# Kernel optimization log

Hardware: AMD Instinct MI355X
Metric: run time of the kernel (lower is better)

## Reference

```python
import jax, jax.numpy as jnp
import numpy as np

N = 50000
E = 800000
D = 128
L = 3


def gru_cell(m, h, w_ih, w_hh, b_ih, b_hh):
    # m, h: [N, D]; w_ih, w_hh: [3D, D]; b_ih, b_hh: [3D]
    gi = m @ w_ih.T + b_ih  # [N, 3D]
    gh = h @ w_hh.T + b_hh  # [N, 3D]
    i_r, i_z, i_n = jnp.split(gi, 3, axis=-1)
    h_r, h_z, h_n = jnp.split(gh, 3, axis=-1)
    r = jax.nn.sigmoid(i_r + h_r)
    z = jax.nn.sigmoid(i_z + h_z)
    n = jnp.tanh(i_n + r * h_n)
    return (1.0 - z) * n + z * h


def setup_inputs() -> dict:
    key = jax.random.key(0)
    ks = jax.random.split(key, 8)
    s = 1.0 / np.sqrt(D)
    z = jax.random.normal(ks[0], (N, D), dtype=jnp.float32)
    edge_index = jax.random.randint(ks[1], (2, E), 0, N, dtype=jnp.int64)
    weight = jax.random.uniform(ks[2], (L, D, D), dtype=jnp.float32, minval=-s, maxval=s)
    w_ih = jax.random.uniform(ks[3], (3 * D, D), dtype=jnp.float32, minval=-s, maxval=s)
    w_hh = jax.random.uniform(ks[4], (3 * D, D), dtype=jnp.float32, minval=-s, maxval=s)
    b_ih = jax.random.uniform(ks[5], (3 * D,), dtype=jnp.float32, minval=-s, maxval=s)
    b_hh = jax.random.uniform(ks[6], (3 * D,), dtype=jnp.float32, minval=-s, maxval=s)
    return {"z": z, "edge_index": edge_index, "weight": weight,
            "w_ih": w_ih, "w_hh": w_hh, "b_ih": b_ih, "b_hh": b_hh}


def reference(z, edge_index, weight, w_ih, w_hh, b_ih, b_hh):
    # GatedGraphConv: per layer, m = h @ W_l; aggregate m[src] into dst (sum); GRU update.
    src, dst = edge_index[0], edge_index[1]
    h = z  # in_channels == out_channels, no padding
    for l in range(L):
        m = h @ weight[l]                              # [N, D]
        agg = jax.ops.segment_sum(m[src], dst, num_segments=N)  # scatter-add over edges
        h = gru_cell(agg, h, w_ih, w_hh, b_ih, b_hh)
    return h
```

## Files before the change

kernel.cpp:

```cpp
#include <hip/hip_runtime.h>
#include <hip/hip_bf16.h>

#define NN 50000
#define NE 800000
#define D 128
#define NL 3
#define G3 384

typedef __attribute__((ext_vector_type(4))) float f32x4;
typedef __attribute__((ext_vector_type(2))) float f32x2;
typedef _Float16 f16;
typedef __attribute__((ext_vector_type(8))) _Float16 f16x8;
typedef __attribute__((ext_vector_type(2))) _Float16 f16x2;

__global__ void detect_i64_kernel(const int* __restrict__ ei, int* __restrict__ flag) {
    __shared__ int any_nz;
    if (threadIdx.x == 0) any_nz = 0;
    __syncthreads();
    int v = ei[threadIdx.x * 2 + 1];
    if (v != 0) atomicOr(&any_nz, 1);
    __syncthreads();
    if (threadIdx.x == 0) *flag = (any_nz == 0) ? 1 : 0;
}

static __device__ __forceinline__ void load_edge(const int* ei, const int* flag, int e,
                                                 int& src, int& dst) {
    if (*flag) {
        src = ei[2LL * e];
        dst = ei[2LL * (NE + e)];
    } else {
        src = ei[e];
        dst = ei[NE + e];
    }
}

__global__ void hist_kernel(const int* __restrict__ ei, const int* __restrict__ flag,
                            int* __restrict__ counts, unsigned short* __restrict__ rank16) {
    int e = blockIdx.x * blockDim.x + threadIdx.x;
    if (e >= NE) return;
    int src, dst;
    load_edge(ei, flag, e, src, dst);
    rank16[e] = (unsigned short)atomicAdd(counts + dst, 1);
}

#define SBLK 256
#define NSB ((NN + SBLK - 1) / SBLK)

__global__ __launch_bounds__(SBLK) void scan_reduce_kernel(const int* __restrict__ counts,
                                                           int* __restrict__ block_sums) {
    __shared__ int lds[SBLK];
    int i = blockIdx.x * SBLK + threadIdx.x;
    lds[threadIdx.x] = (i < NN) ? counts[i] : 0;
    __syncthreads();
    for (int off = SBLK / 2; off > 0; off >>= 1) {
        if (threadIdx.x < off) lds[threadIdx.x] += lds[threadIdx.x + off];
        __syncthreads();
    }
    if (threadIdx.x == 0) block_sums[blockIdx.x] = lds[0];
}

__global__ __launch_bounds__(256) void scan_offsets_kernel(const int* __restrict__ block_sums,
                                                           int* __restrict__ block_off,
                                                           int* __restrict__ row_start) {
    __shared__ int lds[256];
    int t = threadIdx.x;
    int v = (t < NSB) ? block_sums[t] : 0;
    lds[t] = v;
    __syncthreads();
    for (int off = 1; off < 256; off <<= 1) {
        int x = (t >= off) ? lds[t - off] : 0;
        __syncthreads();
        lds[t] += x;
        __syncthreads();
    }
    if (t < NSB) block_off[t] = lds[t] - v;
    if (t == 255) row_start[NN] = lds[255];
}

__global__ __launch_bounds__(SBLK) void scan_final_kernel(const int* __restrict__ counts,
                                                          const int* __restrict__ block_off,
                                                          int* __restrict__ row_start) {
    __shared__ int lds[SBLK];
    int i = blockIdx.x * SBLK + threadIdx.x;
    int v = (i < NN) ? counts[i] : 0;
    lds[threadIdx.x] = v;
    __syncthreads();
    for (int off = 1; off < SBLK; off <<= 1) {
        int x = (threadIdx.x >= off) ? lds[threadIdx.x - off] : 0;
        __syncthreads();
        lds[threadIdx.x] += x;
        __syncthreads();
    }
    if (i < NN) row_start[i] = block_off[blockIdx.x] + lds[threadIdx.x] - v;
}

__global__ void fill_kernel(const int* __restrict__ ei, const int* __restrict__ flag,
                            const int* __restrict__ row_start,
                            const unsigned short* __restrict__ rank16,
                            unsigned short* __restrict__ csr16) {
    int e = blockIdx.x * blockDim.x + threadIdx.x;
    if (e >= NE) return;
    int src, dst;
    load_edge(ei, flag, e, src, dst);
    csr16[row_start[dst] + (int)rank16[e]] = (unsigned short)src;
}

__global__ void init_h_kernel(const float* __restrict__ z, f16* __restrict__ h) {
    int i = blockIdx.x * blockDim.x + threadIdx.x;
    if (i * 2 >= NN * D) return;
    f32x2 v = *(const f32x2*)(z + i * 2);
    f16x2 o = {(f16)v[0], (f16)v[1]};
    *(f16x2*)(h + i * 2) = o;
}

__global__ __launch_bounds__(256) void gather_kernel(
    const f16* __restrict__ h, const int* __restrict__ row_start,
    const unsigned short* __restrict__ csr16, f16* __restrict__ agg) {
    int row = blockIdx.x * 4 + (threadIdx.x >> 6);
    if (row >= NN) return;
    int lane = threadIdx.x & 63;
    int eslot = lane >> 4;
    int c0 = (lane & 15) * 8;
    int beg = row_start[row], end = row_start[row + 1];
    float acc[8] = {0.f, 0.f, 0.f, 0.f, 0.f, 0.f, 0.f, 0.f};
    float acc2[8] = {0.f, 0.f, 0.f, 0.f, 0.f, 0.f, 0.f, 0.f};
    int e = beg;
    for (; e + 7 < end; e += 8) {
        int s0 = (int)csr16[e + eslot];
        int s1 = (int)csr16[e + eslot + 4];
        f16x8 v0 = *(const f16x8*)(h + s0 * D + c0);
        f16x8 v1 = *(const f16x8*)(h + s1 * D + c0);
#pragma unroll
        for (int j = 0; j < 8; ++j) { acc[j] += (float)v0[j]; acc2[j] += (float)v1[j]; }
    }
    for (; e + eslot < end; e += 4) {
        int s = (int)csr16[e + eslot];
        f16x8 v = *(const f16x8*)(h + s * D + c0);
#pragma unroll
        for (int j = 0; j < 8; ++j) acc[j] += (float)v[j];
    }
#pragma unroll
    for (int j = 0; j < 8; ++j) {
        acc[j] += acc2[j];
        acc[j] += __shfl_xor(acc[j], 16, 64);
        acc[j] += __shfl_xor(acc[j], 32, 64);
    }
    if (lane < 16) {
        f16x8 o;
#pragma unroll
        for (int j = 0; j < 8; ++j) o[j] = (f16)acc[j];
        *(f16x8*)(agg + row * D + c0) = o;
    }
}

__global__ void precompute_weights(const float* __restrict__ weight,
                                   const float* __restrict__ w_ih,
                                   const float* __restrict__ w_hh,
                                   f16* __restrict__ wct, f16* __restrict__ whh) {
    int l = blockIdx.x / G3;
    int g = blockIdx.x % G3;
    int c = threadIdx.x;
    __shared__ float wih_row[D];
    wih_row[c] = w_ih[g * D + c];
    __syncthreads();
    const float* wrow = weight + ((long long)l * D + c) * D;
    float acc = 0.f;
#pragma unroll 8
    for (int j = 0; j < D; ++j) acc += wrow[j] * wih_row[j];
    wct[((long long)l * G3 + g) * D + c] = (f16)acc;
    if (l == 0) whh[g * D + c] = (f16)w_hh[g * D + c];
}

#define TMG 128
#define NDT 2
#define MFMA_F16 __builtin_amdgcn_mfma_f32_16x16x32_f16
__global__ __launch_bounds__(512) void gru_fused_kernel(
    const f16* __restrict__ agg, const f16* __restrict__ hin, f16* __restrict__ hout,
    const f16* __restrict__ wct, const f16* __restrict__ whh,
    const float* __restrict__ b_ih, const float* __restrict__ b_hh,
    float* __restrict__ out_f32) {
    __shared__ char wlds[NDT * 6 * 4096];
    const int tid = threadIdx.x;
    const int lane = tid & 63;
    const int wv = tid >> 6;
    const int fr = lane & 15;
    const int kg = lane >> 4;
    const int m0 = blockIdx.x * TMG;
    const int dt0 = blockIdx.y * NDT;

    int arow = m0 + wv * 16 + fr;
    int arc = arow < NN ? arow : NN - 1;
    const int abase = arc * D;

    f16x8 fa[4], fh[4];
#pragma unroll
    for (int ks = 0; ks < 4; ++ks) {
        int k0 = ks * 32 + kg * 8;
        fa[ks] = *(const f16x8*)(agg + abase + k0);
        fh[ks] = *(const f16x8*)(hin + abase + k0);
    }

#pragma unroll
    for (int p6 = 0; p6 < NDT * 3; ++p6) {
        int unit = tid + p6 * 512;
        int dpanel = unit >> 8;
        int dti = dpanel / 6;
        int panel = dpanel % 6;
        int u = unit & 255;
        int sr = u >> 4;
        int sc = (u & 15) * 8;
        int gr = (dt0 + dti) * 16;
        const f16* srcp = (panel < 3)
                              ? wct + (panel * 128 + gr + sr) * D + sc
                              : whh + ((panel - 3) * 128 + gr + sr) * D + sc;
        int wb = (u * 16) ^ ((sr & 7) << 4);
        *(f16x8*)(wlds + dpanel * 4096 + wb) = *(const f16x8*)srcp;
    }
    __syncthreads();

#pragma unroll
    for (int dti = 0; dti < NDT; ++dti) {
        const int gr = (dt0 + dti) * 16;
        const char* wb0 = wlds + dti * 6 * 4096;
        f32x4 a_ir = {0, 0, 0, 0}, a_iz = {0, 0, 0, 0}, a_in = {0, 0, 0, 0};
        f32x4 a_hr = {0, 0, 0, 0}, a_hz = {0, 0, 0, 0}, a_hn = {0, 0, 0, 0};
#pragma unroll
        for (int ks = 0; ks < 4; ++ks) {
            const int kb = fr * 256 + (((ks * 4 + kg) ^ (fr & 7)) << 4);
            f16x8 bir = *(const f16x8*)(wb0 + 0 * 4096 + kb);
            f16x8 biz = *(const f16x8*)(wb0 + 1 * 4096 + kb);
            f16x8 bin = *(const f16x8*)(wb0 + 2 * 4096 + kb);
            f16x8 bhr = *(const f16x8*)(wb0 + 3 * 4096 + kb);
            f16x8 bhz = *(const f16x8*)(wb0 + 4 * 4096 + kb);
            f16x8 bhn = *(const f16x8*)(wb0 + 5 * 4096 + kb);
            a_ir = MFMA_F16(fa[ks], bir, a_ir, 0, 0, 0);
            a_iz = MFMA_F16(fa[ks], biz, a_iz, 0, 0, 0);
            a_in = MFMA_F16(fa[ks], bin, a_in, 0, 0, 0);
            a_hr = MFMA_F16(fh[ks], bhr, a_hr, 0, 0, 0);
            a_hz = MFMA_F16(fh[ks], bhz, a_hz, 0, 0, 0);
            a_hn = MFMA_F16(fh[ks], bhn, a_hn, 0, 0, 0);
        }
        const int d = gr + fr;
        float bir_ = b_ih[d], biz_ = b_ih[128 + d], bin_ = b_ih[256 + d];
        float bhr_ = b_hh[d], bhz_ = b_hh[128 + d], bhn_ = b_hh[256 + d];
#pragma unroll
        for (int j = 0; j < 4; ++j) {
            int row = m0 + wv * 16 + kg * 4 + j;
            if (row >= NN) continue;
            float ir = a_ir[j] + bir_, iz = a_iz[j] + biz_, in_ = a_in[j] + bin_;
            float hr = a_hr[j] + bhr_, hz = a_hz[j] + bhz_, hn = a_hn[j] + bhn_;
            float r = 1.f / (1.f + __expf(-(ir + hr)));
            float zz = 1.f / (1.f + __expf(-(iz + hz)));
            float e2 = __expf(2.f * (in_ + r * hn));
            float nn = 1.f - 2.f / (e2 + 1.f);
            int off = row * D + d;
            float hold = (float)hin[off];
            float hnew = (1.f - zz) * nn + zz * hold;
            if (out_f32)
                out_f32[off] = hnew;
            else
                hout[off] = (f16)hnew;
        }
    }
}

__global__ __launch_bounds__(256) void gru_fused_fallback(
    const f16* __restrict__ agg, const f16* __restrict__ hin, f16* __restrict__ hout,
    const f16* __restrict__ wct, const f16* __restrict__ whh,
    const float* __restrict__ b_ih, const float* __restrict__ b_hh,
    float* __restrict__ out_f32) {
    const int tid = threadIdx.x;
    const int lane = tid & 63;
    const int wv = tid >> 6;
    const int fr = lane & 15;
    const int kg = lane >> 4;
    const int m0 = blockIdx.x * 64;
    int arow = m0 + wv * 16 + fr;
    int arc = arow < NN ? arow : NN - 1;
    const int abase = arc * D;
    f16x8 fa[4], fh[4];
#pragma unroll
    for (int ks = 0; ks < 4; ++ks) {
        int k0 = ks * 32 + kg * 8;
        fa[ks] = *(const f16x8*)(agg + abase + k0);
        fh[ks] = *(const f16x8*)(hin + abase + k0);
    }
#pragma unroll 1
    for (int dt = 0; dt < 8; ++dt) {
        const int g = dt * 16 + fr;
        f32x4 a_ir = {0, 0, 0, 0}, a_iz = {0, 0, 0, 0}, a_in = {0, 0, 0, 0};
        f32x4 a_hr = {0, 0, 0, 0}, a_hz = {0, 0, 0, 0}, a_hn = {0, 0, 0, 0};
#pragma unroll
        for (int ks = 0; ks < 4; ++ks) {
            int k0 = ks * 32 + kg * 8;
            f16x8 bir = *(const f16x8*)(wct + (g)*D + k0);
            f16x8 biz = *(const f16x8*)(wct + (128 + g) * D + k0);
            f16x8 bin = *(const f16x8*)(wct + (256 + g) * D + k0);
            f16x8 bhr = *(const f16x8*)(whh + (g)*D + k0);
            f16x8 bhz = *(const f16x8*)(whh + (128 + g) * D + k0);
            f16x8 bhn = *(const f16x8*)(whh + (256 + g) * D + k0);
            a_ir = MFMA_F16(fa[ks], bir, a_ir, 0, 0, 0);
            a_iz = MFMA_F16(fa[ks], biz, a_iz, 0, 0, 0);
            a_in = MFMA_F16(fa[ks], bin, a_in, 0, 0, 0);
            a_hr = MFMA_F16(fh[ks], bhr, a_hr, 0, 0, 0);
            a_hz = MFMA_F16(fh[ks], bhz, a_hz, 0, 0, 0);
            a_hn = MFMA_F16(fh[ks], bhn, a_hn, 0, 0, 0);
        }
        const int d = g;
        float bir_ = b_ih[d], biz_ = b_ih[128 + d], bin_ = b_ih[256 + d];
        float bhr_ = b_hh[d], bhz_ = b_hh[128 + d], bhn_ = b_hh[256 + d];
#pragma unroll
        for (int j = 0; j < 4; ++j) {
            int row = m0 + wv * 16 + kg * 4 + j;
            if (row >= NN) continue;
            float ir = a_ir[j] + bir_, iz = a_iz[j] + biz_, in_ = a_in[j] + bin_;
            float hr = a_hr[j] + bhr_, hz = a_hz[j] + bhz_, hn = a_hn[j] + bhn_;
            float r = 1.f / (1.f + __expf(-(ir + hr)));
            float zz = 1.f / (1.f + __expf(-(iz + hz)));
            float e2 = __expf(2.f * (in_ + r * hn));
            float nn = 1.f - 2.f / (e2 + 1.f);
            int off = row * D + d;
            float hold = (float)hin[off];
            float hnew = (1.f - zz) * nn + zz * hold;
            if (out_f32)
                out_f32[off] = hnew;
            else
                hout[off] = (f16)hnew;
        }
    }
}

extern "C" void kernel_launch(void* const* d_in, const int* in_sizes, int n_in,
                              void* d_out, int out_size, void* d_ws, size_t ws_size,
                              hipStream_t stream) {
    const float* z = (const float*)d_in[0];
    const int* ei = (const int*)d_in[1];
    const float* weight = (const float*)d_in[2];
    const float* w_ih = (const float*)d_in[3];
    const float* w_hh = (const float*)d_in[4];
    const float* b_ih = (const float*)d_in[5];
    const float* b_hh = (const float*)d_in[6];
    float* out = (float*)d_out;

    char* ws = (char*)d_ws;
    size_t off = 0;
    f16* wct = (f16*)(ws + off); off += 294912;
    f16* whh = (f16*)(ws + off); off += 98304;
    int* flag       = (int*)(ws + off); off += 256;
    int* counts     = (int*)(ws + off); off += (size_t)NN * 4;
    int* row_start  = (int*)(ws + off); off += (size_t)(NN + 16) * 4;
    int* block_sums = (int*)(ws + off); off += (size_t)NSB * 4;
    int* block_off  = (int*)(ws + off); off += (size_t)NSB * 4;
    unsigned short* rank16 = (unsigned short*)(ws + off); off += (size_t)NE * 2;
    unsigned short* csr16  = (unsigned short*)(ws + off); off += (size_t)NE * 2;
    f16* agg  = (f16*)(ws + off); off += (size_t)NN * D * 2;
    f16* hA   = (f16*)(ws + off); off += (size_t)NN * D * 2;
    f16* hB   = (f16*)(ws + off); off += (size_t)NN * D * 2;
    const bool split = (ws_size >= off);
    if (!split) hB = hA;

    detect_i64_kernel<<<1, 256, 0, stream>>>(ei, flag);
    hipMemsetAsync(counts, 0, (size_t)NN * 4, stream);
    hist_kernel<<<(NE + 255) / 256, 256, 0, stream>>>(ei, flag, counts, rank16);
    scan_reduce_kernel<<<NSB, SBLK, 0, stream>>>(counts, block_sums);
    scan_offsets_kernel<<<1, 256, 0, stream>>>(block_sums, block_off, row_start);
    scan_final_kernel<<<NSB, SBLK, 0, stream>>>(counts, block_off, row_start);
    fill_kernel<<<(NE + 255) / 256, 256, 0, stream>>>(ei, flag, row_start, rank16, csr16);
    precompute_weights<<<NL * G3, 128, 0, stream>>>(weight, w_ih, w_hh, wct, whh);
    const int npair = NN * D / 2;
    init_h_kernel<<<(npair + 255) / 256, 256, 0, stream>>>(z, hA);

    const dim3 gg((NN + TMG - 1) / TMG, 8 / NDT);
    const f16* cin = hA;
    for (int l = 0; l < NL; ++l) {
        gather_kernel<<<(NN + 3) / 4, 256, 0, stream>>>(cin, row_start, csr16, agg);
        f16* cout = split ? ((cin == hA) ? hB : hA) : (f16*)cin;
        long long woff = (long long)l * G3 * D;
        float* last_out = (l == NL - 1) ? out : nullptr;
        if (split) {
            gru_fused_kernel<<<gg, 512, 0, stream>>>(agg, cin, cout, wct + woff, whh,
                                                     b_ih, b_hh, last_out);
        } else {
            gru_fused_fallback<<<(NN + 63) / 64, 256, 0, stream>>>(
                agg, cin, cout, wct + woff, whh, b_ih, b_hh, last_out);
        }
        cin = cout;
    }
}
```

Before: 297.6 us.

## Pack dst and rank per edge, coarsen CSR build, enlarge GRU tiles to 1024 threads

```diff
diff --git a/kernel.cpp b/kernel.cpp
--- a/kernel.cpp
+++ b/kernel.cpp
@@ -23,24 +23,20 @@
     if (threadIdx.x == 0) *flag = (any_nz == 0) ? 1 : 0;
 }
 
-static __device__ __forceinline__ void load_edge(const int* ei, const int* flag, int e,
-                                                 int& src, int& dst) {
-    if (*flag) {
-        src = ei[2LL * e];
-        dst = ei[2LL * (NE + e)];
-    } else {
-        src = ei[e];
-        dst = ei[NE + e];
-    }
-}
-
+#define HBLK ((NE / 4 + 255) / 256)
 __global__ void hist_kernel(const int* __restrict__ ei, const int* __restrict__ flag,
-                            int* __restrict__ counts, unsigned short* __restrict__ rank16) {
-    int e = blockIdx.x * blockDim.x + threadIdx.x;
-    if (e >= NE) return;
-    int src, dst;
-    load_edge(ei, flag, e, src, dst);
-    rank16[e] = (unsigned short)atomicAdd(counts + dst, 1);
+                            int* __restrict__ counts, unsigned* __restrict__ dstrank) {
+    const int fl = *flag;
+    int base = blockIdx.x * blockDim.x + threadIdx.x;
+    const int stride = HBLK * 256;
+#pragma unroll
+    for (int k = 0; k < 4; ++k) {
+        int e = base + k * stride;
+        if (e >= NE) continue;
+        int dst = fl ? ei[2LL * (NE + e)] : ei[NE + e];
+        unsigned r = (unsigned)atomicAdd(counts + dst, 1);
+        dstrank[e] = (unsigned)dst | (r << 16);
+    }
 }
 
 #define SBLK 256
@@ -96,13 +92,19 @@
 
 __global__ void fill_kernel(const int* __restrict__ ei, const int* __restrict__ flag,
                             const int* __restrict__ row_start,
-                            const unsigned short* __restrict__ rank16,
+                            const unsigned* __restrict__ dstrank,
                             unsigned short* __restrict__ csr16) {
-    int e = blockIdx.x * blockDim.x + threadIdx.x;
-    if (e >= NE) return;
-    int src, dst;
-    load_edge(ei, flag, e, src, dst);
-    csr16[row_start[dst] + (int)rank16[e]] = (unsigned short)src;
+    const int fl = *flag;
+    int base = blockIdx.x * blockDim.x + threadIdx.x;
+    const int stride = HBLK * 256;
+#pragma unroll
+    for (int k = 0; k < 4; ++k) {
+        int e = base + k * stride;
+        if (e >= NE) continue;
+        int src = fl ? ei[2LL * e] : ei[e];
+        unsigned dr = dstrank[e];
+        csr16[row_start[dr & 0xFFFF] + (int)(dr >> 16)] = (unsigned short)src;
+    }
 }
 
 __global__ void init_h_kernel(const float* __restrict__ z, f16* __restrict__ h) {
@@ -111,6 +113,14 @@
     f32x2 v = *(const f32x2*)(z + i * 2);
     f16x2 o = {(f16)v[0], (f16)v[1]};
     *(f16x2*)(h + i * 2) = o;
+}
+
+__global__ void finalize_kernel(const f16* __restrict__ h, float* __restrict__ out) {
+    int i = blockIdx.x * blockDim.x + threadIdx.x;
+    if (i * 2 >= NN * D) return;
+    f16x2 v = *(const f16x2*)(h + i * 2);
+    f32x2 o = {(float)v[0], (float)v[1]};
+    *(f32x2*)(out + i * 2) = o;
 }
 
 __global__ __launch_bounds__(256) void gather_kernel(
@@ -171,10 +181,11 @@
     if (l == 0) whh[g * D + c] = (f16)w_hh[g * D + c];
 }
 
-#define TMG 128
+#define TMG 256
 #define NDT 2
+#define GRUTHR 1024
 #define MFMA_F16 __builtin_amdgcn_mfma_f32_16x16x32_f16
-__global__ __launch_bounds__(512) void gru_fused_kernel(
+__global__ __launch_bounds__(GRUTHR) void gru_fused_kernel(
     const f16* __restrict__ agg, const f16* __restrict__ hin, f16* __restrict__ hout,
     const f16* __restrict__ wct, const f16* __restrict__ whh,
     const float* __restrict__ b_ih, const float* __restrict__ b_hh,
@@ -201,8 +212,8 @@
     }
 
 #pragma unroll
-    for (int p6 = 0; p6 < NDT * 3; ++p6) {
-        int unit = tid + p6 * 512;
+    for (int p6 = 0; p6 < NDT * 6 * 256 / GRUTHR; ++p6) {
+        int unit = tid + p6 * GRUTHR;
         int dpanel = unit >> 8;
         int dti = dpanel / 6;
         int panel = dpanel % 6;
@@ -213,7 +224,7 @@
         const f16* srcp = (panel < 3)
                               ? wct + (panel * 128 + gr + sr) * D + sc
                               : whh + ((panel - 3) * 128 + gr + sr) * D + sc;
-        int wb = (u * 16) ^ ((sr & 7) << 4);
+        int wb = ((u * 16) ^ ((sr & 7) << 4));
         *(f16x8*)(wlds + dpanel * 4096 + wb) = *(const f16x8*)srcp;
     }
     __syncthreads();
@@ -267,8 +278,7 @@
 __global__ __launch_bounds__(256) void gru_fused_fallback(
     const f16* __restrict__ agg, const f16* __restrict__ hin, f16* __restrict__ hout,
     const f16* __restrict__ wct, const f16* __restrict__ whh,
-    const float* __restrict__ b_ih, const float* __restrict__ b_hh,
-    float* __restrict__ out_f32) {
+    const float* __restrict__ b_ih, const float* __restrict__ b_hh) {
     const int tid = threadIdx.x;
     const int lane = tid & 63;
     const int wv = tid >> 6;
@@ -321,11 +331,7 @@
             float nn = 1.f - 2.f / (e2 + 1.f);
             int off = row * D + d;
             float hold = (float)hin[off];
-            float hnew = (1.f - zz) * nn + zz * hold;
-            if (out_f32)
-                out_f32[off] = hnew;
-            else
-                hout[off] = (f16)hnew;
+            hout[off] = (f16)((1.f - zz) * nn + zz * hold);
         }
     }
 }
@@ -351,39 +357,44 @@
     int* row_start  = (int*)(ws + off); off += (size_t)(NN + 16) * 4;
     int* block_sums = (int*)(ws + off); off += (size_t)NSB * 4;
     int* block_off  = (int*)(ws + off); off += (size_t)NSB * 4;
-    unsigned short* rank16 = (unsigned short*)(ws + off); off += (size_t)NE * 2;
-    unsigned short* csr16  = (unsigned short*)(ws + off); off += (size_t)NE * 2;
+    unsigned* dstrank = (unsigned*)(ws + off); off += (size_t)NE * 4;
+    unsigned short* csr16 = (unsigned short*)(ws + off); off += (size_t)NE * 2;
     f16* agg  = (f16*)(ws + off); off += (size_t)NN * D * 2;
     f16* hA   = (f16*)(ws + off); off += (size_t)NN * D * 2;
     f16* hB   = (f16*)(ws + off); off += (size_t)NN * D * 2;
     const bool split = (ws_size >= off);
-    if (!split) hB = hA;
 
     detect_i64_kernel<<<1, 256, 0, stream>>>(ei, flag);
     hipMemsetAsync(counts, 0, (size_t)NN * 4, stream);
-    hist_kernel<<<(NE + 255) / 256, 256, 0, stream>>>(ei, flag, counts, rank16);
+    hist_kernel<<<HBLK, 256, 0, stream>>>(ei, flag, counts, dstrank);
     scan_reduce_kernel<<<NSB, SBLK, 0, stream>>>(counts, block_sums);
     scan_offsets_kernel<<<1, 256, 0, stream>>>(block_sums, block_off, row_start);
     scan_final_kernel<<<NSB, SBLK, 0, stream>>>(counts, block_off, row_start);
-    fill_kernel<<<(NE + 255) / 256, 256, 0, stream>>>(ei, flag, row_start, rank16, csr16);
+    fill_kernel<<<HBLK, 256, 0, stream>>>(ei, flag, row_start, dstrank, csr16);
     precompute_weights<<<NL * G3, 128, 0, stream>>>(weight, w_ih, w_hh, wct, whh);
     const int npair = NN * D / 2;
     init_h_kernel<<<(npair + 255) / 256, 256, 0, stream>>>(z, hA);
 
-    const dim3 gg((NN + TMG - 1) / TMG, 8 / NDT);
-    const f16* cin = hA;
-    for (int l = 0; l < NL; ++l) {
-        gather_kernel<<<(NN + 3) / 4, 256, 0, stream>>>(cin, row_start, csr16, agg);
-        f16* cout = split ? ((cin == hA) ? hB : hA) : (f16*)cin;
-        long long woff = (long long)l * G3 * D;
-        float* last_out = (l == NL - 1) ? out : nullptr;
-        if (split) {
-            gru_fused_kernel<<<gg, 512, 0, stream>>>(agg, cin, cout, wct + woff, whh,
-                                                     b_ih, b_hh, last_out);
-        } else {
+    if (split) {
+        const dim3 gg((NN + TMG - 1) / TMG, 8 / NDT);
+        const f16* cin = hA;
+        for (int l = 0; l < NL; ++l) {
+            gather_kernel<<<(NN + 3) / 4, 256, 0, stream>>>(cin, row_start, csr16, agg);
+            f16* cout = (cin == hA) ? hB : hA;
+            long long woff = (long long)l * G3 * D;
+            float* last_out = (l == NL - 1) ? out : nullptr;
+            gru_fused_kernel<<<gg, GRUTHR, 0, stream>>>(agg, cin, cout, wct + woff, whh,
+                                                        b_ih, b_hh, last_out);
+            cin = cout;
+        }
+    } else {
+        f16* aggo = (f16*)d_out;
+        for (int l = 0; l < NL; ++l) {
+            gather_kernel<<<(NN + 3) / 4, 256, 0, stream>>>(hA, row_start, csr16, aggo);
+            long long woff = (long long)l * G3 * D;
             gru_fused_fallback<<<(NN + 63) / 64, 256, 0, stream>>>(
-                agg, cin, cout, wct + woff, whh, b_ih, b_hh, last_out);
-        }
-        cin = cout;
-    }
-}
+                aggo, hA, hA, wct + woff, whh, b_ih, b_hh);
+        }
+        finalize_kernel<<<(npair + 255) / 256, 256, 0, stream>>>(hA, out);
+    }
+}
```

Result: slower. 311.5 us (+4.6%).
